# Optimization experiments

Hardware: AMD Instinct MI355X
Metric: run time of the kernel (lower is better)

## Reference

```python
import jax, jax.numpy as jnp
import numpy as np

DIM = 1024
INTER = 1024
N_EXPERTS = 16
TOPK = 4
SHARED_INTER = 2 * INTER  # n_shared_experts * moe_inter_dim
T = 8192


def setup_inputs() -> dict:
    key = jax.random.key(0)
    ks = jax.random.split(key, 15)
    s = 0.02
    inp = {
        "x": jax.random.normal(ks[0], (T, DIM), jnp.float32),
        "gate_w": jax.random.normal(ks[1], (N_EXPERTS, DIM), jnp.float32) * s,
        # routed experts, stacked over expert axis
        "ew1": jax.random.normal(ks[2], (N_EXPERTS, INTER, DIM), jnp.float32) * s,
        "eb1": jax.random.normal(ks[3], (N_EXPERTS, INTER), jnp.float32) * s,
        "ew2": jax.random.normal(ks[4], (N_EXPERTS, DIM, INTER), jnp.float32) * s,
        "eb2": jax.random.normal(ks[5], (N_EXPERTS, DIM), jnp.float32) * s,
        "ew3": jax.random.normal(ks[6], (N_EXPERTS, INTER, DIM), jnp.float32) * s,
        "eb3": jax.random.normal(ks[7], (N_EXPERTS, INTER), jnp.float32) * s,
        # shared expert MLP (inter = 2 * moe_inter_dim)
        "sw1": jax.random.normal(ks[8], (SHARED_INTER, DIM), jnp.float32) * s,
        "sb1": jax.random.normal(ks[9], (SHARED_INTER,), jnp.float32) * s,
        "sw2": jax.random.normal(ks[10], (DIM, SHARED_INTER), jnp.float32) * s,
        "sb2": jax.random.normal(ks[11], (DIM,), jnp.float32) * s,
        "sw3": jax.random.normal(ks[12], (SHARED_INTER, DIM), jnp.float32) * s,
        "sb3": jax.random.normal(ks[13], (SHARED_INTER,), jnp.float32) * s,
    }
    return inp


def _ffn(x, w1, b1, w2, b2, w3, b3):
    # w2(silu(w1(x)) * w3(x))
    return (jax.nn.silu(x @ w1.T + b1) * (x @ w3.T + b3)) @ w2.T + b2


def reference(x, gate_w, ew1, eb1, ew2, eb2, ew3, eb3, sw1, sb1, sw2, sb2, sw3, sb3):
    # Gate: softmax scores in fp32 (n_groups=1 -> no group masking), top-k routing
    scores = jax.nn.softmax((x @ gate_w.T).astype(jnp.float32), axis=-1)  # [T, E]
    top_vals, idx = jax.lax.top_k(scores, TOPK)  # [T, K]
    weights = top_vals.astype(x.dtype)  # route_scale = 1.0, softmax score_func

    # Per-expert combine weight: zero for unselected experts.
    nT = x.shape[0]
    cw = jnp.zeros((nT, N_EXPERTS), x.dtype).at[
        jnp.arange(nT)[:, None], idx
    ].add(weights)  # [T, E]

    # Routed experts: masked-dense dispatch (weight 0 kills unselected terms)
    y = jnp.zeros_like(x)
    for e in range(N_EXPERTS):
        y = y + cw[:, e:e + 1] * _ffn(x, ew1[e], eb1[e], ew2[e], eb2[e], ew3[e], eb3[e])

    # Shared experts (always applied)
    z = _ffn(x, sw1, sb1, sw2, sb2, sw3, sb3)
    return y + z
```

## Files before the change

### kernel.cpp

```cpp
#include <hip/hip_runtime.h>
#include <cstdint>
#include <cstddef>

#define TOK     8192
#define DIMD    1024
#define INTERD  1024
#define NEXP    16
#define SINTER  2048
#define CAP256  36864
#define MAXT    144
#define HBLK    32

typedef __bf16 bf16_t;
typedef __bf16 bf16x8_t __attribute__((ext_vector_type(8)));
typedef __bf16 bf16x4_t __attribute__((ext_vector_type(4)));
typedef float  f32x4_t  __attribute__((ext_vector_type(4)));

__device__ __forceinline__ void gload_lds16(const bf16_t* g, bf16_t* l) {
  __builtin_amdgcn_global_load_lds((const __attribute__((address_space(1))) void*)g,
                                   (__attribute__((address_space(3))) void*)l,
                                   16, 0, 0);
}

#define SBAR __builtin_amdgcn_sched_barrier(0)

__global__ void init_kernel(int* toklist, float* wtlist, int* tile_e, int* tile_rs) {
  int i = blockIdx.x * blockDim.x + threadIdx.x;
  if (i < CAP256) { toklist[i] = -1; wtlist[i] = 0.0f; }
  if (i < 512)    { tile_e[i] = -1; tile_rs[i] = 0; }
}

__global__ void cvt_kernel(const float* __restrict__ in, bf16_t* __restrict__ out, int n4) {
  int stride = gridDim.x * blockDim.x;
  for (int i = blockIdx.x * blockDim.x + threadIdx.x; i < n4; i += stride) {
    float4 v = ((const float4*)in)[i];
    bf16x4_t o;
    o[0] = (bf16_t)v.x; o[1] = (bf16_t)v.y; o[2] = (bf16_t)v.z; o[3] = (bf16_t)v.w;
    ((bf16x4_t*)out)[i] = o;
  }
}

__global__ void cvt_ileave(const float* __restrict__ s1, const float* __restrict__ s3,
                           bf16_t* __restrict__ dst, int total4, int esh) {
  int stride = gridDim.x * blockDim.x;
  int fmask = (1 << esh) - 1;
  for (int i = blockIdx.x * blockDim.x + threadIdx.x; i < total4; i += stride) {
    int k4 = i & 255;
    int fr = i >> 8;
    int e  = fr >> esh;
    int f  = fr & fmask;
    int p  = f >> 4, s = f & 15;
    int real = ((p >> 1) << 4) + s;
    size_t srow = ((size_t)e << (esh - 1)) + real;
    const float* src = ((p & 1) ? s3 : s1) + (srow << 10) + (k4 << 2);
    float4 v = *(const float4*)src;
    bf16x4_t o;
    o[0] = (bf16_t)v.x; o[1] = (bf16_t)v.y; o[2] = (bf16_t)v.z; o[3] = (bf16_t)v.w;
    ((bf16x4_t*)dst)[i] = o;
  }
}

__global__ __launch_bounds__(256)
void gate_kernel(const float* __restrict__ x, const float* __restrict__ gw,
                 int* __restrict__ tkidx, float* __restrict__ tkwt) {
  int wv = threadIdx.x >> 6, lane = threadIdx.x & 63;
  int t = blockIdx.x * 4 + wv;
  const float4* xp = (const float4*)(x + (size_t)t * DIMD + lane * 16);
  float4 xv[4];
#pragma unroll
  for (int i = 0; i < 4; ++i) xv[i] = xp[i];
  float sc[NEXP];
#pragma unroll
  for (int e = 0; e < NEXP; ++e) {
    const float4* wp = (const float4*)(gw + (size_t)e * DIMD + lane * 16);
    float s = 0.0f;
#pragma unroll
    for (int i = 0; i < 4; ++i) {
      float4 w = wp[i];
      s += xv[i].x * w.x + xv[i].y * w.y + xv[i].z * w.z + xv[i].w * w.w;
    }
    sc[e] = s;
  }
#pragma unroll
  for (int off = 32; off > 0; off >>= 1)
#pragma unroll
    for (int e = 0; e < NEXP; ++e)
      sc[e] += __shfl_xor(sc[e], off, 64);
  if (lane == 0) {
    float m = sc[0];
#pragma unroll
    for (int e = 1; e < NEXP; ++e) m = fmaxf(m, sc[e]);
    float p[NEXP], s = 0.0f;
#pragma unroll
    for (int e = 0; e < NEXP; ++e) { p[e] = __expf(sc[e] - m); s += p[e]; }
    float inv = 1.0f / s;
    unsigned used = 0;
    for (int k = 0; k < 4; ++k) {
      int best = 0; float bv = -1.0f;
#pragma unroll
      for (int e = 0; e < NEXP; ++e)
        if (!((used >> e) & 1u) && p[e] > bv) { bv = p[e]; best = e; }
      used |= 1u << best;
      tkidx[t * 4 + k] = best;
      tkwt[t * 4 + k] = bv * inv;
    }
  }
}

__global__ __launch_bounds__(256)
void hist_kernel(const int* __restrict__ tkidx, int* __restrict__ blkhist) {
  __shared__ int h[NEXP];
  if (threadIdx.x < NEXP) h[threadIdx.x] = 0;
  __syncthreads();
  int4 v = ((const int4*)tkidx)[blockIdx.x * 256 + threadIdx.x];
  atomicAdd(&h[v.x], 1);
  atomicAdd(&h[v.y], 1);
  atomicAdd(&h[v.z], 1);
  atomicAdd(&h[v.w], 1);
  __syncthreads();
  if (threadIdx.x < NEXP) blkhist[blockIdx.x * NEXP + threadIdx.x] = h[threadIdx.x];
}

__global__ void offs_kernel(const int* __restrict__ blkhist, int* __restrict__ offsets,
                            int* __restrict__ blkbase,
                            int* __restrict__ tile_e, int* __restrict__ tile_rs) {
  if (threadIdx.x != 0 || blockIdx.x != 0) return;
  int counts[NEXP];
  for (int e = 0; e < NEXP; ++e) {
    int s = 0;
    for (int b = 0; b < HBLK; ++b) s += blkhist[b * NEXP + e];
    counts[e] = s;
  }
  int off = 0, nt = 0;
  for (int e = 0; e < NEXP; ++e) {
    offsets[e] = off;
    int c = counts[e];
    int ntile = (c + 255) >> 8;
    for (int i = 0; i < ntile; ++i) { tile_e[nt] = e; tile_rs[nt] = off + (i << 8); ++nt; }
    off += ntile << 8;
  }
  offsets[NEXP] = off;
  for (int e = 0; e < NEXP; ++e) {
    int base = offsets[e];
    for (int b = 0; b < HBLK; ++b) {
      blkbase[b * NEXP + e] = base;
      base += blkhist[b * NEXP + e];
    }
  }
}

__global__ __launch_bounds__(256)
void scat_kernel(const int* __restrict__ tkidx, const float* __restrict__ tkwt,
                 const int* __restrict__ blkbase,
                 int* __restrict__ toklist, float* __restrict__ wtlist,
                 int4* __restrict__ pos4) {
  __shared__ int cur[NEXP];
  if (threadIdx.x < NEXP) cur[threadIdx.x] = blkbase[blockIdx.x * NEXP + threadIdx.x];
  __syncthreads();
  int idx = blockIdx.x * 256 + threadIdx.x;
  int4 v = ((const int4*)tkidx)[idx];
  float4 w = ((const float4*)tkwt)[idx];
  int p0 = atomicAdd(&cur[v.x], 1); toklist[p0] = idx; wtlist[p0] = w.x;
  int p1 = atomicAdd(&cur[v.y], 1); toklist[p1] = idx; wtlist[p1] = w.y;
  int p2 = atomicAdd(&cur[v.z], 1); toklist[p2] = idx; wtlist[p2] = w.z;
  int p3 = atomicAdd(&cur[v.w], 1); toklist[p3] = idx; wtlist[p3] = w.w;
  pos4[idx] = make_int4(p0, p1, p2, p3);
}

__global__ __launch_bounds__(256)
void fuse_kernel(const int4* __restrict__ pos4, const bf16_t* __restrict__ Yg,
                 float* __restrict__ out) {
  int t = blockIdx.x;
  int4 p = pos4[t];
  int c = threadIdx.x;
  float4 o = ((const float4*)(out + (size_t)t * DIMD))[c];
  bf16x4_t y0 = ((const bf16x4_t*)(Yg + (size_t)p.x * DIMD))[c];
  bf16x4_t y1 = ((const bf16x4_t*)(Yg + (size_t)p.y * DIMD))[c];
  bf16x4_t y2 = ((const bf16x4_t*)(Yg + (size_t)p.z * DIMD))[c];
  bf16x4_t y3 = ((const bf16x4_t*)(Yg + (size_t)p.w * DIMD))[c];
  o.x += (float)y0[0] + (float)y1[0] + (float)y2[0] + (float)y3[0];
  o.y += (float)y0[1] + (float)y1[1] + (float)y2[1] + (float)y3[1];
  o.z += (float)y0[2] + (float)y1[2] + (float)y2[2] + (float)y3[2];
  o.w += (float)y0[3] + (float)y1[3] + (float)y2[3] + (float)y3[3];
  ((float4*)(out + (size_t)t * DIMD))[c] = o;
}

template <int BM, bool TABLE, int EPI>
__global__ __launch_bounds__(512, 2)
void gemm8p(const bf16_t* __restrict__ Ag, const bf16_t* __restrict__ Bw,
            const float* __restrict__ bias1, const float* __restrict__ bias3,
            void* __restrict__ Outp,
            const int* __restrict__ tile_e, const int* __restrict__ tile_rs,
            const int* __restrict__ toklist, const float* __restrict__ wtlist,
            int K, int ldOut, size_t strideB, int biasStride) {
  constexpr int BN = 256;
  constexpr int AH = BM / 128;
  constexpr int MI = BM / 32;
  constexpr int ABYTES = BM * 128;
  constexpr int BUFB = ABYTES + 32768;
  __shared__ __align__(16) bf16_t lds[BUFB];

  int rowstart, e = 0;
  if constexpr (TABLE) {
    e = tile_e[blockIdx.y];
    if (e < 0) return;
    rowstart = tile_rs[blockIdx.y];
  } else {
    rowstart = blockIdx.y * BM;
  }
  const bf16_t* Bwp = Bw + (TABLE ? (size_t)e * strideB : (size_t)0);
  const int boff = TABLE ? e * biasStride : 0;

  const int tid = threadIdx.x, lane = tid & 63, wv = tid >> 6;
  const int wm = wv >> 2, wn = wv & 3;
  const int xsw = (lane & 7) << 4;
  const int klo = (lane >> 4) * 16;

  const bf16_t* srcpA[4];
  const bf16_t* srcpB[4];
#pragma unroll
  for (int h = 0; h < AH; ++h)
#pragma unroll
    for (int j = 0; j < 2; ++j) {
      int idx = tid + j * 512;
      int r = h * 128 + (idx >> 3);
      int slot = (idx & 7) ^ ((idx >> 3) & 7);
      long arow;
      if constexpr (TABLE && EPI == 0) {
        int t = toklist[rowstart + r];
        arow = (t < 0) ? 0 : t;
      } else {
        arow = rowstart + r;
      }
      srcpA[h * 2 + j] = Ag + (size_t)arow * K + slot * 8;
    }
#pragma unroll
  for (int h = 0; h < 2; ++h)
#pragma unroll
    for (int j = 0; j < 2; ++j) {
      int idx = tid + j * 512;
      int r = h * 128 + (idx >> 3);
      int slot = (idx & 7) ^ ((idx >> 3) & 7);
      srcpB[h * 2 + j] = Bwp + (size_t)((int)blockIdx.x * BN + r) * K + slot * 8;
    }

#define STG_A(H, NB, KT) do {                                                    \
    bf16_t* d_ = (bf16_t*)lds + ((NB) * BUFB + (H) * 16384) / 2 + tid * 8;       \
    gload_lds16(srcpA[(H) * 2 + 0] + (KT) * 64, d_);                             \
    gload_lds16(srcpA[(H) * 2 + 1] + (KT) * 64, d_ + 4096);                      \
  } while (0)
#define STG_B(H, NB, KT) do {                                                    \
    bf16_t* d_ = (bf16_t*)lds + ((NB) * BUFB + ABYTES + (H) * 16384) / 2 + tid * 8; \
    gload_lds16(srcpB[(H) * 2 + 0] + (KT) * 64, d_);                             \
    gload_lds16(srcpB[(H) * 2 + 1] + (KT) * 64, d_ + 4096);                      \
  } while (0)

  f32x4_t acc[MI][4] = {};
  bf16x8_t bfr[4];

#define PHASE(KS, MH, STG, WT, BUFP, NB, KT1) do {                               \
    bf16x8_t afr[4];                                                             \
    _Pragma("unroll")                                                            \
    for (int q = 0; q < 4; ++q) {                                                \
      int rl = wm * 64 + q * 16 + (lane & 15);                                   \
      afr[q] = *(const bf16x8_t*)((BUFP) + (MH) * 16384 +                        \
                 ((rl * 128 + (KS) * 64 + klo) ^ xsw));                          \
    }                                                                            \
    if ((MH) == 0) {                                                             \
      _Pragma("unroll")                                                          \
      for (int ni = 0; ni < 4; ++ni) {                                           \
        int ct = wn * 64 + ni * 16 + (lane & 15);                                \
        bfr[ni] = *(const bf16x8_t*)((BUFP) + ABYTES + (ct >> 7) * 16384 +       \
                   (((ct & 127) * 128 + (KS) * 64 + klo) ^ xsw));                \
      }                                                                          \
    }                                                                            \
    if ((STG) == 1) { STG_A(0, NB, KT1); STG_B(0, NB, KT1); STG_B(1, NB, KT1); } \
    else if ((STG) == 2) { STG_A(1, NB, KT1); }                                  \
    SBAR;                                                                        \
    if ((WT) == 1) asm volatile("s_waitcnt vmcnt(6)" ::: "memory");              \
    else if ((WT) == 2) asm volatile("s_waitcnt vmcnt(2)" ::: "memory");         \
    else if ((WT) == 3) asm volatile("s_waitcnt vmcnt(0)" ::: "memory");         \
    SBAR;                                                                        \
    __builtin_amdgcn_s_barrier();                                                \
    asm volatile("s_waitcnt lgkmcnt(0)" ::: "memory");                           \
    SBAR;                                                                        \
    __builtin_amdgcn_s_setprio(1);                                               \
    _Pragma("unroll")                                                            \
    for (int q = 0; q < 4; ++q)                                                  \
      _Pragma("unroll")                                                          \
      for (int ni = 0; ni < 4; ++ni)                                             \
        acc[(MH) * 4 + q][ni] = __builtin_amdgcn_mfma_f32_16x16x32_bf16(         \
            afr[q], bfr[ni], acc[(MH) * 4 + q][ni], 0, 0, 0);                    \
    __builtin_amdgcn_s_setprio(0);                                               \
    __builtin_amdgcn_s_barrier();                                                \
    SBAR;                                                                        \
  } while (0)

  const int NTK = K >> 6;

  STG_A(0, 0, 0);
  STG_B(0, 0, 0);
  STG_B(1, 0, 0);
  if constexpr (AH == 2) STG_A(1, 0, 0);
  SBAR;
  asm volatile("s_waitcnt vmcnt(0)" ::: "memory");
  SBAR;
  __builtin_amdgcn_s_barrier();
  SBAR;

  if constexpr (BM == 256) {
    for (int kt = 0; kt < NTK - 1; ++kt) {
      const char* bufp = (const char*)lds + (kt & 1) * BUFB;
      int nb = (kt + 1) & 1, k1 = kt + 1;
      PHASE(0, 0, 1, 1, bufp, nb, k1);
      PHASE(0, 1, 2, 0, bufp, nb, k1);
      PHASE(1, 0, 0, 0, bufp, nb, k1);
      PHASE(1, 1, 0, 2, bufp, nb, k1);
    }
    const char* bufp = (const char*)lds + ((NTK - 1) & 1) * BUFB;
    PHASE(0, 0, 0, 3, bufp, 0, 0);
    PHASE(0, 1, 0, 0, bufp, 0, 0);
    PHASE(1, 0, 0, 0, bufp, 0, 0);
    PHASE(1, 1, 0, 0, bufp, 0, 0);
  } else {
    for (int kt = 0; kt < NTK; ++kt) {
      const char* bufp = (const char*)lds + (kt & 1) * BUFB;
      int nb = (kt + 1) & 1, k1 = kt + 1;
      int stg = (kt + 1 < NTK) ? 1 : 0;
      PHASE(0, 0, stg, 0, bufp, nb, k1);
      PHASE(1, 0, 0, 3, bufp, nb, k1);
    }
  }

  if constexpr (EPI == 0) {
    float b1v[2], b3v[2];
    int rcbase = (int)blockIdx.x * 128 + wn * 32 + (lane & 15);
#pragma unroll
    for (int ni2 = 0; ni2 < 2; ++ni2) {
      b1v[ni2] = bias1[boff + rcbase + ni2 * 16];
      b3v[ni2] = bias3[boff + rcbase + ni2 * 16];
    }
    bf16_t* Hout = (bf16_t*)Outp;
#pragma unroll
    for (int mi = 0; mi < MI; ++mi)
#pragma unroll
      for (int rg = 0; rg < 4; ++rg) {
        int Rb = ((mi >= 4) ? 128 : 0) + wm * 64 + (mi & 3) * 16;
        int rt = Rb + ((lane >> 4) << 2) + rg;
        int grow = rowstart + rt;
        float wt = 1.0f;
        if constexpr (TABLE) wt = wtlist[grow];
        size_t ob = (size_t)grow * ldOut + rcbase;
#pragma unroll
        for (int ni2 = 0; ni2 < 2; ++ni2) {
          float v1 = acc[mi][2 * ni2][rg] + b1v[ni2];
          float v3 = acc[mi][2 * ni2 + 1][rg] + b3v[ni2];
          float sg = v1 / (1.0f + __expf(-v1));
          Hout[ob + ni2 * 16] = (bf16_t)(sg * v3 * wt);
        }
      }
  } else if constexpr (EPI == 1) {
    float bv[4];
    int colbase = (int)blockIdx.x * BN + wn * 64 + (lane & 15);
#pragma unroll
    for (int ni = 0; ni < 4; ++ni) bv[ni] = bias1[boff + colbase + ni * 16];
    bf16_t* Yout = (bf16_t*)Outp;
#pragma unroll
    for (int mi = 0; mi < MI; ++mi)
#pragma unroll
      for (int rg = 0; rg < 4; ++rg) {
        int Rb = ((mi >= 4) ? 128 : 0) + wm * 64 + (mi & 3) * 16;
        int rt = Rb + ((lane >> 4) << 2) + rg;
        int grow = rowstart + rt;
        float wt = wtlist[grow];
        size_t ob = (size_t)grow * ldOut + colbase;
#pragma unroll
        for (int ni = 0; ni < 4; ++ni)
          Yout[ob + ni * 16] = (bf16_t)(acc[mi][ni][rg] + wt * bv[ni]);
      }
  } else {
    float bv[4];
    int colbase = (int)blockIdx.x * BN + wn * 64 + (lane & 15);
#pragma unroll
    for (int ni = 0; ni < 4; ++ni) bv[ni] = bias1[boff + colbase + ni * 16];
    float* Fout = (float*)Outp;
#pragma unroll
    for (int mi = 0; mi < MI; ++mi)
#pragma unroll
      for (int rg = 0; rg < 4; ++rg) {
        int Rb = ((mi >= 4) ? 128 : 0) + wm * 64 + (mi & 3) * 16;
        int rt = Rb + ((lane >> 4) << 2) + rg;
        int grow = rowstart + rt;
        size_t ob = (size_t)grow * ldOut + colbase;
#pragma unroll
        for (int ni = 0; ni < 4; ++ni)
          Fout[ob + ni * 16] = acc[mi][ni][rg] + bv[ni];
      }
  }
#undef PHASE
#undef STG_A
#undef STG_B
}

extern "C" void kernel_launch(void* const* d_in, const int* in_sizes, int n_in,
                              void* d_out, int out_size, void* d_ws, size_t ws_size,
                              hipStream_t stream) {
  const float* x   = (const float*)d_in[0];
  const float* gw  = (const float*)d_in[1];
  const float* ew1 = (const float*)d_in[2];
  const float* eb1 = (const float*)d_in[3];
  const float* ew2 = (const float*)d_in[4];
  const float* eb2 = (const float*)d_in[5];
  const float* ew3 = (const float*)d_in[6];
  const float* eb3 = (const float*)d_in[7];
  const float* sw1 = (const float*)d_in[8];
  const float* sb1 = (const float*)d_in[9];
  const float* sw2 = (const float*)d_in[10];
  const float* sb2 = (const float*)d_in[11];
  const float* sw3 = (const float*)d_in[12];
  const float* sb3 = (const float*)d_in[13];
  float* out = (float*)d_out;
  (void)ws_size;

  char* ws = (char*)d_ws;
  size_t off = 0;
  auto alloc = [&](size_t bytes) -> void* {
    off = (off + 255) & ~(size_t)255;
    void* p = ws + off;
    off += bytes;
    return p;
  };

  bf16_t* xb    = (bf16_t*)alloc((size_t)TOK * DIMD * 2);
  bf16_t* ew13i = (bf16_t*)alloc((size_t)NEXP * 2 * INTERD * DIMD * 2);
  bf16_t* ew2b  = (bf16_t*)alloc((size_t)NEXP * DIMD * INTERD * 2);
  bf16_t* sw13i = (bf16_t*)alloc((size_t)2 * SINTER * DIMD * 2);
  bf16_t* sw2b  = (bf16_t*)alloc((size_t)DIMD * SINTER * 2);
  bf16_t* Hun   = (bf16_t*)alloc((size_t)CAP256 * INTERD * 2);
  bf16_t* Hs    = Hun;
  bf16_t* Hg    = Hun;
  bf16_t* Yg    = xb;
  int*   toklist = (int*)alloc(CAP256 * 4);
  float* wtlist  = (float*)alloc(CAP256 * 4);
  int*   offsets = (int*)alloc((NEXP + 1) * 4);
  int*   blkhist = (int*)alloc(HBLK * NEXP * 4);
  int*   blkbase = (int*)alloc(HBLK * NEXP * 4);
  int*   tile_e  = (int*)alloc(512 * 4);
  int*   tile_rs = (int*)alloc(512 * 4);
  int*   tkidx   = (int*)alloc((size_t)TOK * 4 * 4);
  float* tkwt    = (float*)alloc((size_t)TOK * 4 * 4);
  int4*  pos4    = (int4*)alloc((size_t)TOK * 16);

  init_kernel<<<(CAP256 + 255) / 256, 256, 0, stream>>>(toklist, wtlist, tile_e, tile_rs);

  cvt_kernel<<<2048, 256, 0, stream>>>(x,   xb,   TOK * DIMD / 4);
  cvt_kernel<<<2048, 256, 0, stream>>>(ew2, ew2b, NEXP * DIMD * INTERD / 4);
  cvt_kernel<<<512,  256, 0, stream>>>(sw2, sw2b, DIMD * SINTER / 4);
  cvt_ileave<<<2048, 256, 0, stream>>>(ew1, ew3, ew13i, NEXP * 2 * INTERD * DIMD / 4, 11);
  cvt_ileave<<<1024, 256, 0, stream>>>(sw1, sw3, sw13i, 2 * SINTER * DIMD / 4, 12);

  gate_kernel<<<TOK / 4, 256, 0, stream>>>(x, gw, tkidx, tkwt);
  hist_kernel<<<HBLK, 256, 0, stream>>>(tkidx, blkhist);
  offs_kernel<<<1, 64, 0, stream>>>(blkhist, offsets, blkbase, tile_e, tile_rs);
  scat_kernel<<<HBLK, 256, 0, stream>>>(tkidx, tkwt, blkbase, toklist, wtlist, pos4);

  gemm8p<256, false, 0><<<dim3(2 * SINTER / 256, TOK / 256), 512, 0, stream>>>(
      xb, sw13i, sb1, sb3, Hs, nullptr, nullptr, nullptr, nullptr,
      DIMD, SINTER, 0, 0);
  gemm8p<128, false, 2><<<dim3(DIMD / 256, TOK / 128), 512, 0, stream>>>(
      Hs, sw2b, sb2, nullptr, out, nullptr, nullptr, nullptr, nullptr,
      SINTER, DIMD, 0, 0);

  gemm8p<256, true, 0><<<dim3(2 * INTERD / 256, MAXT), 512, 0, stream>>>(
      xb, ew13i, eb1, eb3, Hg, tile_e, tile_rs, toklist, wtlist,
      DIMD, INTERD, (size_t)2 * INTERD * DIMD, INTERD);
  gemm8p<256, true, 1><<<dim3(DIMD / 256, MAXT), 512, 0, stream>>>(
      Hg, ew2b, eb2, nullptr, Yg, tile_e, tile_rs, toklist, wtlist,
      INTERD, DIMD, (size_t)DIMD * INTERD, DIMD);

  fuse_kernel<<<TOK, 256, 0, stream>>>(pos4, Yg, out);
}
```

Measured before the change: 558.0 us.

## Swizzle GEMM workgroup order across XCDs and merge conversion launches

Remaps the linear workgroup index so consecutive hardware-dispatched blocks, which go round-robin across the 8 XCDs, land on contiguous tiles. The intent is better L2 reuse of A and B tiles within each XCD. It also fuses three fp32-to-bf16 conversion launches into one kernel to cut launch overhead. The remap assumes the grid size is divisible by 8; if it is not, some tiles could be skipped or computed twice.

```diff
diff --git a/kernel.cpp b/kernel.cpp
--- a/kernel.cpp
+++ b/kernel.cpp
@@ -30,13 +30,20 @@
   if (i < 512)    { tile_e[i] = -1; tile_rs[i] = 0; }
 }
 
-__global__ void cvt_kernel(const float* __restrict__ in, bf16_t* __restrict__ out, int n4) {
+__global__ void cvt3_kernel(const float* __restrict__ s0, bf16_t* __restrict__ d0, int n0,
+                            const float* __restrict__ s1, bf16_t* __restrict__ d1, int n1,
+                            const float* __restrict__ s2, bf16_t* __restrict__ d2, int n2) {
+  int total = n0 + n1 + n2;
   int stride = gridDim.x * blockDim.x;
-  for (int i = blockIdx.x * blockDim.x + threadIdx.x; i < n4; i += stride) {
-    float4 v = ((const float4*)in)[i];
+  for (int i = blockIdx.x * blockDim.x + threadIdx.x; i < total; i += stride) {
+    const float* s; bf16_t* d; int j = i;
+    if (j < n0) { s = s0; d = d0; }
+    else if ((j - n0) < n1) { j -= n0; s = s1; d = d1; }
+    else { j -= n0 + n1; s = s2; d = d2; }
+    float4 v = ((const float4*)s)[j];
     bf16x4_t o;
     o[0] = (bf16_t)v.x; o[1] = (bf16_t)v.y; o[2] = (bf16_t)v.z; o[3] = (bf16_t)v.w;
-    ((bf16x4_t*)out)[i] = o;
+    ((bf16x4_t*)d)[j] = o;
   }
 }
 
@@ -200,13 +207,19 @@
   constexpr int BUFB = ABYTES + 32768;
   __shared__ __align__(16) bf16_t lds[BUFB];
 
+  int nwg = (int)(gridDim.x * gridDim.y);
+  int lin = (int)(blockIdx.y * gridDim.x + blockIdx.x);
+  int sw = (lin & 7) * (nwg >> 3) + (lin >> 3);
+  int bx = sw % (int)gridDim.x;
+  int by = sw / (int)gridDim.x;
+
   int rowstart, e = 0;
   if constexpr (TABLE) {
-    e = tile_e[blockIdx.y];
+    e = tile_e[by];
     if (e < 0) return;
-    rowstart = tile_rs[blockIdx.y];
+    rowstart = tile_rs[by];
   } else {
-    rowstart = blockIdx.y * BM;
+    rowstart = by * BM;
   }
   const bf16_t* Bwp = Bw + (TABLE ? (size_t)e * strideB : (size_t)0);
   const int boff = TABLE ? e * biasStride : 0;
@@ -241,7 +254,7 @@
       int idx = tid + j * 512;
       int r = h * 128 + (idx >> 3);
       int slot = (idx & 7) ^ ((idx >> 3) & 7);
-      srcpB[h * 2 + j] = Bwp + (size_t)((int)blockIdx.x * BN + r) * K + slot * 8;
+      srcpB[h * 2 + j] = Bwp + (size_t)(bx * BN + r) * K + slot * 8;
     }
 
 #define STG_A(H, NB, KT) do {                                                    \
@@ -334,7 +347,7 @@
 
   if constexpr (EPI == 0) {
     float b1v[2], b3v[2];
-    int rcbase = (int)blockIdx.x * 128 + wn * 32 + (lane & 15);
+    int rcbase = bx * 128 + wn * 32 + (lane & 15);
 #pragma unroll
     for (int ni2 = 0; ni2 < 2; ++ni2) {
       b1v[ni2] = bias1[boff + rcbase + ni2 * 16];
@@ -361,7 +374,7 @@
       }
   } else if constexpr (EPI == 1) {
     float bv[4];
-    int colbase = (int)blockIdx.x * BN + wn * 64 + (lane & 15);
+    int colbase = bx * BN + wn * 64 + (lane & 15);
 #pragma unroll
     for (int ni = 0; ni < 4; ++ni) bv[ni] = bias1[boff + colbase + ni * 16];
     bf16_t* Yout = (bf16_t*)Outp;
@@ -380,7 +393,7 @@
       }
   } else {
     float bv[4];
-    int colbase = (int)blockIdx.x * BN + wn * 64 + (lane & 15);
+    int colbase = bx * BN + wn * 64 + (lane & 15);
 #pragma unroll
     for (int ni = 0; ni < 4; ++ni) bv[ni] = bias1[boff + colbase + ni * 16];
     float* Fout = (float*)Outp;
@@ -453,9 +466,9 @@
 
   init_kernel<<<(CAP256 + 255) / 256, 256, 0, stream>>>(toklist, wtlist, tile_e, tile_rs);
 
-  cvt_kernel<<<2048, 256, 0, stream>>>(x,   xb,   TOK * DIMD / 4);
-  cvt_kernel<<<2048, 256, 0, stream>>>(ew2, ew2b, NEXP * DIMD * INTERD / 4);
-  cvt_kernel<<<512,  256, 0, stream>>>(sw2, sw2b, DIMD * SINTER / 4);
+  cvt3_kernel<<<2048, 256, 0, stream>>>(x, xb, TOK * DIMD / 4,
+                                        ew2, ew2b, NEXP * DIMD * INTERD / 4,
+                                        sw2, sw2b, DIMD * SINTER / 4);
   cvt_ileave<<<2048, 256, 0, stream>>>(ew1, ew3, ew13i, NEXP * 2 * INTERD * DIMD / 4, 11);
   cvt_ileave<<<1024, 256, 0, stream>>>(sw1, sw3, sw13i, 2 * SINTER * DIMD / 4, 12);
 
```

After: 548.4 us. Within noise of the previous version (-1.7%).
